# Optimization experiments

Hardware: AMD Instinct MI355X
Metric: run time of the kernel (lower is better)

Reference implementation:

```python
import jax, jax.numpy as jnp
import numpy as np

LOG2PI = float(np.log(2.0 * np.pi))


def setup_inputs() -> dict:
    key = jax.random.key(0)
    ks = jax.random.split(key, 5)
    B, T, XD, C = 128, 2050, 6, 64
    return {
        "x": jax.random.normal(ks[0], (B, T, XD), jnp.float32),
        "observation_means": jax.random.uniform(ks[1], (C, XD), dtype=jnp.float32),
        "observation_stddevs": jax.random.uniform(ks[2], (C, XD), dtype=jnp.float32),
        "log_A": jax.random.normal(ks[3], (C, C), jnp.float32),
        "log_pi": jax.random.normal(ks[4], (C,), jnp.float32),
    }


def _emission_logprob(x, means, stds):
    # Normal(means[:, :4], relu(stds[:, :4]) + 0.1).log_prob(x[:, :, :4]) summed over feat dim
    mu = means[:, :4]                       # (C,4)
    sigma = jax.nn.relu(stds[:, :4]) + 0.1  # (C,4)
    z = (x[:, :, None, :4] - mu) / sigma    # (B,T,C,4)
    return jnp.sum(-0.5 * z * z - jnp.log(sigma) - 0.5 * LOG2PI, axis=-1)  # (B,T,C)


def _forward_scalers(logp, log_A, log_pi):
    # scaled HMM forward pass; returns per-step log normalizers (T,B)
    a0 = logp[:, 0] + log_pi
    s0 = jax.nn.logsumexp(a0, axis=-1)
    a0n = a0 - s0[:, None]

    def step(a_prev, lp_t):
        a = lp_t + jax.nn.logsumexp(a_prev[:, :, None] + log_A[None], axis=1)
        s = jax.nn.logsumexp(a, axis=-1)
        return a - s[:, None], s

    _, s_rest = jax.lax.scan(step, a0n, jnp.swapaxes(logp[:, 1:], 0, 1))
    return jnp.concatenate([s0[None], s_rest], axis=0)  # (T,B)


def _viterbi(logp, log_A, log_pi):
    d0 = logp[:, 0] + log_pi  # (B,C)

    def step(d_prev, lp_t):
        scores = d_prev[:, :, None] + log_A[None]  # (B,C_prev,C_cur)
        psi_t = jnp.argmax(scores, axis=1)
        d = jnp.max(scores, axis=1) + lp_t
        return d, psi_t

    d_last, psi = jax.lax.scan(step, d0, jnp.swapaxes(logp[:, 1:], 0, 1))  # psi: (T-1,B,C)
    c_last = jnp.argmax(d_last, axis=-1)  # (B,)

    def back(c_next, psi_t):
        c_t = jnp.take_along_axis(psi_t, c_next[:, None], axis=1)[:, 0]
        return c_t, c_t

    _, cs = jax.lax.scan(back, c_last, psi, reverse=True)  # (T-1,B)
    c = jnp.concatenate([cs, c_last[None]], axis=0)  # (T,B)
    return jnp.swapaxes(c, 0, 1)  # (B,T)


def reference(x, observation_means, observation_stddevs, log_A, log_pi):
    logA = jax.nn.log_softmax(log_A, axis=1)
    logpi = jax.nn.log_softmax(log_pi, axis=0)
    logp = _emission_logprob(x, observation_means, observation_stddevs)  # (B,T,C)
    scalers = _forward_scalers(logp, logA, logpi)                         # (T,B)
    logp_x = jnp.sum(scalers, axis=0)                                     # (B,)
    c_est = _viterbi(logp, logA, logpi)                                   # (B,T) int
    return logp_x, c_est
```

## Files before the change

### kernel.cpp

```cpp
#include <hip/hip_runtime.h>

#define T_LEN 2050
#define B_SZ 128
#define NCHUNK 33
#define HL2PI 0.91893853320467274178f

__device__ __forceinline__ float waveMax(float v) {
#pragma unroll
    for (int off = 32; off >= 1; off >>= 1)
        v = fmaxf(v, __shfl_xor(v, off, 64));
    return v;
}
__device__ __forceinline__ float waveSum(float v) {
#pragma unroll
    for (int off = 32; off >= 1; off >>= 1)
        v += __shfl_xor(v, off, 64);
    return v;
}
__device__ __forceinline__ void waveArgmax(float& v, int& idx) {
#pragma unroll
    for (int off = 32; off >= 1; off >>= 1) {
        float ov = __shfl_xor(v, off, 64);
        int   oi = __shfl_xor(idx, off, 64);
        if (ov > v || (ov == v && oi < idx)) { v = ov; idx = oi; }
    }
}
__device__ __forceinline__ void cfence() { asm volatile("" ::: "memory"); }

__device__ __forceinline__ float rl(float v, int lane) {
    return __int_as_float(__builtin_amdgcn_readlane(__float_as_int(v), lane));
}

__device__ __forceinline__ float dppSumAll(float v) {
#define SSTEP(ctrl) { int t_ = __builtin_amdgcn_update_dpp(0, __float_as_int(v), ctrl, 0xf, 0xf, true); \
                      v = v + __int_as_float(t_); }
    SSTEP(0x111) SSTEP(0x112) SSTEP(0x114) SSTEP(0x118) SSTEP(0x142) SSTEP(0x143)
#undef SSTEP
    return __int_as_float(__builtin_amdgcn_readlane(__float_as_int(v), 63));
}
__device__ __forceinline__ float dppMaxAll(float v) {
#define MSTEP(ctrl) { int t_ = __builtin_amdgcn_update_dpp(__float_as_int(v), __float_as_int(v), ctrl, 0xf, 0xf, false); \
                      v = fmaxf(v, __int_as_float(t_)); }
    MSTEP(0x111) MSTEP(0x112) MSTEP(0x114) MSTEP(0x118) MSTEP(0x142) MSTEP(0x143)
#undef MSTEP
    return __int_as_float(__builtin_amdgcn_readlane(__float_as_int(v), 63));
}

extern "C" __global__ __launch_bounds__(64, 1)
void hmm_prep(const float* __restrict__ logA_in,
              const float* __restrict__ logpi_in,
              float* __restrict__ lAg,
              float* __restrict__ lpig)
{
    __shared__ float la[64 * 65];
    __shared__ float rowlse[64];
    const int j = threadIdx.x;
#pragma unroll
    for (int k = 0; k < 64; ++k)
        la[k * 65 + j] = logA_in[k * 64 + j];
    cfence();
    {
        float m = -1e30f;
#pragma unroll
        for (int k = 0; k < 64; ++k) m = fmaxf(m, la[j * 65 + k]);
        float s = 0.f;
#pragma unroll
        for (int k = 0; k < 64; ++k) s += expf(la[j * 65 + k] - m);
        rowlse[j] = m + logf(s);
    }
    cfence();
    {
        float v = logpi_in[j];
        float m = waveMax(v);
        float s = waveSum(expf(v - m));
        lpig[j] = v - (m + logf(s));
    }
    float4* o = (float4*)lAg;
#pragma unroll
    for (int k = 0; k < 16; ++k) {
        float4 v;
        v.x = la[(4 * k + 0) * 65 + j] - rowlse[4 * k + 0];
        v.y = la[(4 * k + 1) * 65 + j] - rowlse[4 * k + 1];
        v.z = la[(4 * k + 2) * 65 + j] - rowlse[4 * k + 2];
        v.w = la[(4 * k + 3) * 65 + j] - rowlse[4 * k + 3];
        o[j * 16 + k] = v;
    }
}

extern "C" __global__ __launch_bounds__(256)
void hmm_emis(const float* __restrict__ x,
              const float* __restrict__ means,
              const float* __restrict__ stds,
              float* __restrict__ buf,
              float* __restrict__ m_pre)
{
    const int wid = blockIdx.x * 4 + (threadIdx.x >> 6);
    const int j = threadIdx.x & 63;
    const int t = wid >> 7;
    const int b = wid & 127;

    const float* xt = x + ((size_t)b * T_LEN + t) * 6;
    float x0 = xt[0], x1 = xt[1], x2 = xt[2], x3 = xt[3];

    float mu0 = means[j * 6 + 0], mu1 = means[j * 6 + 1];
    float mu2 = means[j * 6 + 2], mu3 = means[j * 6 + 3];
    float sg0 = fmaxf(stds[j * 6 + 0], 0.f) + 0.1f;
    float sg1 = fmaxf(stds[j * 6 + 1], 0.f) + 0.1f;
    float sg2 = fmaxf(stds[j * 6 + 2], 0.f) + 0.1f;
    float sg3 = fmaxf(stds[j * 6 + 3], 0.f) + 0.1f;
    float ls0 = logf(sg0), ls1 = logf(sg1), ls2 = logf(sg2), ls3 = logf(sg3);

    float z0 = (x0 - mu0) / sg0, z1 = (x1 - mu1) / sg1;
    float z2 = (x2 - mu2) / sg2, z3 = (x3 - mu3) / sg3;
    float e0 = ((-0.5f * z0) * z0 - ls0) - HL2PI;
    float e1 = ((-0.5f * z1) * z1 - ls1) - HL2PI;
    float e2 = ((-0.5f * z2) * z2 - ls2) - HL2PI;
    float e3 = ((-0.5f * z3) * z3 - ls3) - HL2PI;
    float lp = ((e0 + e1) + e2) + e3;

    buf[((size_t)b * T_LEN + t) * 64 + j] = lp;
    float mm = waveMax(lp);
    if (j == 0) m_pre[(size_t)b * T_LEN + t] = mm;
}

#define VIT_REDUCE(SRC)                                                   \
    float m0 = -3.4e38f, m1 = -3.4e38f, m2 = -3.4e38f, m3 = -3.4e38f;     \
    _Pragma("unroll")                                                     \
    for (int gq = 0; gq < 4; ++gq) {                                      \
        float s_[16];                                                     \
        _Pragma("unroll")                                                 \
        for (int m_ = 0; m_ < 16; ++m_) s_[m_] = rl((SRC), 16 * gq + m_); \
        __builtin_amdgcn_sched_barrier(0);                                \
        _Pragma("unroll")                                                 \
        for (int k2 = 0; k2 < 4; k2 += 2) {                               \
            const int ia = 16 * gq + 4 * k2;                              \
            const int ib = ia + 4;                                        \
            float a0_ = s_[4*k2+0] + lA[ia+0], b0_ = s_[4*k2+4] + lA[ib+0]; \
            float a1_ = s_[4*k2+1] + lA[ia+1], b1_ = s_[4*k2+5] + lA[ib+1]; \
            float a2_ = s_[4*k2+2] + lA[ia+2], b2_ = s_[4*k2+6] + lA[ib+2]; \
            float a3_ = s_[4*k2+3] + lA[ia+3], b3_ = s_[4*k2+7] + lA[ib+3]; \
            m0 = fmaxf(fmaxf(m0, a0_), b0_);                              \
            m1 = fmaxf(fmaxf(m1, a1_), b1_);                              \
            m2 = fmaxf(fmaxf(m2, a2_), b2_);                              \
            m3 = fmaxf(fmaxf(m3, a3_), b3_);                              \
        }                                                                 \
    }

extern "C" __global__ __launch_bounds__(64, 1)
void hmm_main(const float* __restrict__ x,
              const float* __restrict__ means,
              const float* __restrict__ stds,
              const float* __restrict__ lAg,
              const float* __restrict__ lpig,
              float* __restrict__ out,
              float* __restrict__ buf,
              const float* __restrict__ m_pre,
              int* __restrict__ c_last)
{
    __shared__ __align__(16) float xs[12304];

    const int j   = threadIdx.x;
    const int bid = blockIdx.x;
    const bool is_fwd = (bid < B_SZ);
    const int b = is_fwd ? bid : bid - B_SZ;

    float lpi = lpig[j];

    if (is_fwd) {
        {
            const float4* xg4 = (const float4*)(x + (size_t)b * T_LEN * 6);
            float4* xs4 = (float4*)xs;
            for (int i = j; i < 3075; i += 64) xs4[i] = xg4[i];
        }
        float mu0 = means[j * 6 + 0], mu1 = means[j * 6 + 1];
        float mu2 = means[j * 6 + 2], mu3 = means[j * 6 + 3];
        float sg0 = fmaxf(stds[j * 6 + 0], 0.f) + 0.1f;
        float sg1 = fmaxf(stds[j * 6 + 1], 0.f) + 0.1f;
        float sg2 = fmaxf(stds[j * 6 + 2], 0.f) + 0.1f;
        float sg3 = fmaxf(stds[j * 6 + 3], 0.f) + 0.1f;
        float ls0 = logf(sg0), ls1 = logf(sg1), ls2 = logf(sg2), ls3 = logf(sg3);
        float i0 = 1.f / sg0, i1 = 1.f / sg1, i2 = 1.f / sg2, i3 = 1.f / sg3;
        float cst = -(ls0 + ls1 + ls2 + ls3) - 4.f * HL2PI;

        float Ac[64];
        {
            const float4* g = (const float4*)lAg;
#pragma unroll
            for (int k = 0; k < 16; ++k) {
                float4 v = g[j * 16 + k];
                Ac[4 * k + 0] = __expf(v.x); Ac[4 * k + 1] = __expf(v.y);
                Ac[4 * k + 2] = __expf(v.z); Ac[4 * k + 3] = __expf(v.w);
            }
        }
        cfence();

        float z0 = (xs[0] - mu0) * i0, z1 = (xs[1] - mu1) * i1;
        float z2 = (xs[2] - mu2) * i2, z3 = (xs[3] - mu3) * i3;
        float a0 = (cst - 0.5f * (z0 * z0 + z1 * z1 + z2 * z2 + z3 * z3)) + lpi;
        float m0a = dppMaxAll(a0);
        float u = __expf(a0 - m0a);
        float s0 = dppSumAll(u);
        double acc = (double)(m0a + __logf(s0));
        u *= (1.0f / s0);

        const float* mp = m_pre + (size_t)b * T_LEN;
        float g0 = mp[1], g1 = mp[2], g2 = mp[3], g3 = mp[4];

#pragma unroll 1
        for (int t = 1; t < T_LEN; ++t) {
            float mm_c = g0; g0 = g1; g1 = g2; g2 = g3;
            int tp = t + 4; if (tp > T_LEN - 1) tp = T_LEN - 1;
            g3 = mp[tp];

            int o = t * 6;
            float y0 = xs[o], y1 = xs[o + 1], y2 = xs[o + 2], y3 = xs[o + 3];
            float w0 = (y0 - mu0) * i0, w1 = (y1 - mu1) * i1;
            float w2 = (y2 - mu2) * i2, w3 = (y3 - mu3) * i3;
            float lp = cst - 0.5f * (w0 * w0 + w1 * w1 + w2 * w2 + w3 * w3);
            float e_c = __expf(lp - mm_c);

            float q0 = 0.f, q1 = 0.f, q2 = 0.f, q3 = 0.f;
#pragma unroll
            for (int gq = 0; gq < 4; ++gq) {
                float s[16];
#pragma unroll
                for (int m = 0; m < 16; ++m) s[m] = rl(u, 16 * gq + m);
#pragma unroll
                for (int k2 = 0; k2 < 4; ++k2) {
                    const int i = 16 * gq + 4 * k2;
                    q0 = fmaf(s[4 * k2 + 0], Ac[i + 0], q0);
                    q1 = fmaf(s[4 * k2 + 1], Ac[i + 1], q1);
                    q2 = fmaf(s[4 * k2 + 2], Ac[i + 2], q2);
                    q3 = fmaf(s[4 * k2 + 3], Ac[i + 3], q3);
                }
            }
            u = ((q0 + q1) + (q2 + q3)) * e_c;
            acc += (double)mm_c;
            if ((t & 3) == 0) {
                float ss = dppSumAll(u);
                acc += (double)__logf(ss);
                u *= (1.0f / ss);
            }
        }
        float sf = dppSumAll(u);
        acc += (double)__logf(sf);
        if (j == 0) out[b] = (float)acc;
    } else {
        float lA[64];
        {
            const float4* g = (const float4*)lAg;
#pragma unroll
            for (int k = 0; k < 16; ++k) {
                float4 v = g[j * 16 + k];
                lA[4 * k + 0] = v.x; lA[4 * k + 1] = v.y;
                lA[4 * k + 2] = v.z; lA[4 * k + 3] = v.w;
            }
        }
        float* bb = buf + (size_t)b * T_LEN * 64 + j;

        float dn = bb[0] + lpi;
        float lr[8];
#pragma unroll
        for (int i = 0; i < 8; ++i) lr[i] = bb[(size_t)(1 + i) * 64];
        bb[0] = dn;

#pragma unroll 1
        for (int tb = 1; tb <= 2033; tb += 8) {
#pragma unroll
            for (int q = 0; q < 8; ++q) {
                const int t = tb + q;
                float lp_c = lr[q];
                lr[q] = bb[(size_t)(t + 8) * 64];
                VIT_REDUCE(dn);
                dn = fmaxf(fmaxf(m0, m1), fmaxf(m2, m3)) + lp_c;
                bb[(size_t)t * 64] = dn;
            }
        }
        float l_last = bb[(size_t)2049 * 64];
#pragma unroll
        for (int q = 0; q < 8; ++q) {
            const int t = 2041 + q;
            float lp_c = lr[q];
            VIT_REDUCE(dn);
            dn = fmaxf(fmaxf(m0, m1), fmaxf(m2, m3)) + lp_c;
            bb[(size_t)t * 64] = dn;
        }
        {
            float lp_c = l_last;
            VIT_REDUCE(dn);
            dn = fmaxf(fmaxf(m0, m1), fmaxf(m2, m3)) + lp_c;
        }

        float vv = dn; int idx = j;
        waveArgmax(vv, idx);
        if (j == 0) c_last[b] = idx;
    }
}

extern "C" __global__ __launch_bounds__(256)
void hmm_psi(const float* __restrict__ buf,
             const float* __restrict__ lAg,
             unsigned char* __restrict__ psi)
{
    __shared__ __align__(16) float sd[4][64];
    const int warp = threadIdx.x >> 6;
    const int j = threadIdx.x & 63;
    const int wid = blockIdx.x * 4 + warp;

    float lA[64];
    {
        const float4* g = (const float4*)lAg;
#pragma unroll
        for (int k = 0; k < 16; ++k) {
            float4 v = g[j * 16 + k];
            lA[4 * k + 0] = v.x; lA[4 * k + 1] = v.y;
            lA[4 * k + 2] = v.z; lA[4 * k + 3] = v.w;
        }
    }
    const float4* dv = (const float4*)sd[warp];
    const int NP = 2049 * B_SZ;

    for (int p = wid; p < NP; p += 8192) {
        const int t = (p >> 7) + 1;
        const int b = p & 127;
        float dval = buf[((size_t)b * T_LEN + (t - 1)) * 64 + j];
        sd[warp][j] = dval;

        float bv0 = -3.4e38f, bv1 = -3.4e38f, bv2 = -3.4e38f, bv3 = -3.4e38f;
        int bi0 = 0, bi1 = 1, bi2 = 2, bi3 = 3;
#pragma unroll
        for (int k = 0; k < 16; ++k) {
            float4 dd = dv[k];
            float v0 = dd.x + lA[4 * k + 0];
            float v1 = dd.y + lA[4 * k + 1];
            float v2 = dd.z + lA[4 * k + 2];
            float v3 = dd.w + lA[4 * k + 3];
            if (v0 > bv0) { bv0 = v0; bi0 = 4 * k + 0; }
            if (v1 > bv1) { bv1 = v1; bi1 = 4 * k + 1; }
            if (v2 > bv2) { bv2 = v2; bi2 = 4 * k + 2; }
            if (v3 > bv3) { bv3 = v3; bi3 = 4 * k + 3; }
        }
        float best = bv0; int bidx = bi0;
        if (bv1 > best || (bv1 == best && bi1 < bidx)) { best = bv1; bidx = bi1; }
        if (bv2 > best || (bv2 == best && bi2 < bidx)) { best = bv2; bidx = bi2; }
        if (bv3 > best || (bv3 == best && bi3 < bidx)) { best = bv3; bidx = bi3; }

        psi[((size_t)t * B_SZ + b) * 64 + j] = (unsigned char)bidx;
    }
}

extern "C" __global__ __launch_bounds__(256)
void hmm_compose(const unsigned char* __restrict__ psi,
                 unsigned char* __restrict__ mt)
{
    const int w = blockIdx.x * 4 + (threadIdx.x >> 6);
    const int j = threadIdx.x & 63;
    const int g = w % NCHUNK;
    const int b = w / NCHUNK;
    const int e = (g < NCHUNK - 1) ? g * 64 + 64 : (T_LEN - 1);
    int M = j;
    for (int t = e; t >= g * 64 + 1; --t)
        M = psi[((size_t)t * B_SZ + b) * 64 + M];
    mt[((size_t)g * B_SZ + b) * 64 + j] = (unsigned char)M;
}

extern "C" __global__ __launch_bounds__(64, 1)
void hmm_fill(const unsigned char* __restrict__ psi,
              const unsigned char* __restrict__ mt,
              const int* __restrict__ c_last,
              float* __restrict__ out)
{
    __shared__ int sb[NCHUNK];
    const int b = blockIdx.x;
    const int g = threadIdx.x;
    const int cl = c_last[b];
    if (g == 0) {
        int cur = cl;
        for (int q = NCHUNK - 1; q >= 0; --q) {
            cur = mt[((size_t)q * B_SZ + b) * 64 + cur];
            sb[q] = cur;
        }
    }
    cfence();
    float* oc = out + B_SZ + (size_t)b * T_LEN;
    if (g == NCHUNK) {
        oc[T_LEN - 1] = (float)cl;
    } else if (g < NCHUNK) {
        const int e = (g < NCHUNK - 1) ? g * 64 + 64 : (T_LEN - 1);
        int s = (g < NCHUNK - 1) ? sb[g + 1] : cl;
        for (int t = e; t >= g * 64 + 1; --t) {
            s = psi[((size_t)t * B_SZ + b) * 64 + s];
            oc[t - 1] = (float)s;
        }
    }
}

extern "C" void kernel_launch(void* const* d_in, const int* in_sizes, int n_in,
                              void* d_out, int out_size, void* d_ws, size_t ws_size,
                              hipStream_t stream)
{
    const float* x      = (const float*)d_in[0];
    const float* means  = (const float*)d_in[1];
    const float* stds   = (const float*)d_in[2];
    const float* logA   = (const float*)d_in[3];
    const float* logpi  = (const float*)d_in[4];
    float* out = (float*)d_out;

    char* base = (char*)d_ws;
    float*         buf   = (float*)base;
    unsigned char* psi   = (unsigned char*)(base + 67174400);
    float*         m_pre = (float*)(base + 67174400);
    unsigned char* mt    = (unsigned char*)(base + 83968000);
    int*           cl    = (int*)(base + 84238336);
    float*         lAg   = (float*)(base + 84238848);
    float*         lpig  = (float*)(base + 84255232);

    hipLaunchKernelGGL(hmm_prep, dim3(1), dim3(64), 0, stream, logA, logpi, lAg, lpig);
    hipLaunchKernelGGL(hmm_emis, dim3((T_LEN * B_SZ) / 4), dim3(256), 0, stream,
                       x, means, stds, buf, m_pre);
    hipLaunchKernelGGL(hmm_main, dim3(2 * B_SZ), dim3(64), 0, stream,
                       x, means, stds, lAg, lpig, out, buf, m_pre, cl);
    hipLaunchKernelGGL(hmm_psi, dim3(2048), dim3(256), 0, stream, buf, lAg, psi);
    hipLaunchKernelGGL(hmm_compose, dim3((NCHUNK * B_SZ) / 4), dim3(256), 0, stream, psi, mt);
    hipLaunchKernelGGL(hmm_fill, dim3(B_SZ), dim3(64), 0, stream, psi, mt, cl, out);
}
```

Baseline: 993.6 us.

## Replace dependent psi gathers with register prefetch and cross-lane permutes in backtrace

The backtrace compose and fill kernels no longer chase pointers through global memory. Each lane now prefetches its own coalesced psi row eight steps ahead and follows the chain with ds_bpermute or readlane, so the dependent global-load latency is taken off the critical path. Chunk-boundary resolution moves into a separate hmm_bound kernel that uses readlane over the composed maps. Fill is spread across one wave per chunk instead of one thread per chunk. This adds a kernel launch, and sbg reuses the start of the workspace buffer, which is no longer needed at that point.

```diff
diff --git a/kernel.cpp b/kernel.cpp
--- a/kernel.cpp
+++ b/kernel.cpp
@@ -357,41 +357,78 @@
     const int j = threadIdx.x & 63;
     const int g = w % NCHUNK;
     const int b = w / NCHUNK;
-    const int e = (g < NCHUNK - 1) ? g * 64 + 64 : (T_LEN - 1);
+    const int e  = (g < NCHUNK - 1) ? g * 64 + 64 : (T_LEN - 1);
+    const int t0 = g * 64 + 1;
+
     int M = j;
-    for (int t = e; t >= g * 64 + 1; --t)
-        M = psi[((size_t)t * B_SZ + b) * 64 + M];
+    int r[8];
+#pragma unroll
+    for (int i = 0; i < 8; ++i) {
+        int t = e - i;
+        r[i] = (t >= t0) ? (int)psi[((size_t)t * B_SZ + b) * 64 + j] : 0;
+    }
+#pragma unroll 1
+    for (int t = e; t >= t0; --t) {
+        const int q = (e - t) & 7;
+        int row = r[q];
+        int tn = t - 8;
+        r[q] = (tn >= t0) ? (int)psi[((size_t)tn * B_SZ + b) * 64 + j] : 0;
+        M = __builtin_amdgcn_ds_bpermute(M << 2, row);
+    }
     mt[((size_t)g * B_SZ + b) * 64 + j] = (unsigned char)M;
 }
 
 extern "C" __global__ __launch_bounds__(64, 1)
+void hmm_bound(const unsigned char* __restrict__ mt,
+               const int* __restrict__ c_last,
+               int* __restrict__ sbg)
+{
+    const int b = blockIdx.x;
+    const int j = threadIdx.x;
+    int rows[NCHUNK];
+#pragma unroll
+    for (int q = 0; q < NCHUNK; ++q)
+        rows[q] = (int)mt[((size_t)q * B_SZ + b) * 64 + j];
+    int cur = c_last[b];
+#pragma unroll
+    for (int q = NCHUNK - 1; q >= 0; --q) {
+        cur = __builtin_amdgcn_readlane(rows[q], cur);
+        if (j == 0) sbg[b * NCHUNK + q] = cur;
+    }
+}
+
+extern "C" __global__ __launch_bounds__(256)
 void hmm_fill(const unsigned char* __restrict__ psi,
-              const unsigned char* __restrict__ mt,
+              const int* __restrict__ sbg,
               const int* __restrict__ c_last,
               float* __restrict__ out)
 {
-    __shared__ int sb[NCHUNK];
-    const int b = blockIdx.x;
-    const int g = threadIdx.x;
+    const int w = blockIdx.x * 4 + (threadIdx.x >> 6);
+    const int j = threadIdx.x & 63;
+    const int g = w % NCHUNK;
+    const int b = w / NCHUNK;
     const int cl = c_last[b];
-    if (g == 0) {
-        int cur = cl;
-        for (int q = NCHUNK - 1; q >= 0; --q) {
-            cur = mt[((size_t)q * B_SZ + b) * 64 + cur];
-            sb[q] = cur;
-        }
-    }
-    cfence();
     float* oc = out + B_SZ + (size_t)b * T_LEN;
-    if (g == NCHUNK) {
-        oc[T_LEN - 1] = (float)cl;
-    } else if (g < NCHUNK) {
-        const int e = (g < NCHUNK - 1) ? g * 64 + 64 : (T_LEN - 1);
-        int s = (g < NCHUNK - 1) ? sb[g + 1] : cl;
-        for (int t = e; t >= g * 64 + 1; --t) {
-            s = psi[((size_t)t * B_SZ + b) * 64 + s];
-            oc[t - 1] = (float)s;
-        }
+
+    const int e  = (g < NCHUNK - 1) ? g * 64 + 64 : (T_LEN - 1);
+    const int t0 = g * 64 + 1;
+    int s = (g < NCHUNK - 1) ? sbg[b * NCHUNK + g + 1] : cl;
+    if (g == NCHUNK - 1 && j == 0) oc[T_LEN - 1] = (float)cl;
+
+    int r[8];
+#pragma unroll
+    for (int i = 0; i < 8; ++i) {
+        int t = e - i;
+        r[i] = (t >= t0) ? (int)psi[((size_t)t * B_SZ + b) * 64 + j] : 0;
+    }
+#pragma unroll 1
+    for (int t = e; t >= t0; --t) {
+        const int q = (e - t) & 7;
+        int row = r[q];
+        int tn = t - 8;
+        r[q] = (tn >= t0) ? (int)psi[((size_t)tn * B_SZ + b) * 64 + j] : 0;
+        s = __builtin_amdgcn_readlane(row, s);
+        if (j == 0) oc[t - 1] = (float)s;
     }
 }
 
@@ -414,6 +451,7 @@
     int*           cl    = (int*)(base + 84238336);
     float*         lAg   = (float*)(base + 84238848);
     float*         lpig  = (float*)(base + 84255232);
+    int*           sbg   = (int*)base;
 
     hipLaunchKernelGGL(hmm_prep, dim3(1), dim3(64), 0, stream, logA, logpi, lAg, lpig);
     hipLaunchKernelGGL(hmm_emis, dim3((T_LEN * B_SZ) / 4), dim3(256), 0, stream,
@@ -422,5 +460,6 @@
                        x, means, stds, lAg, lpig, out, buf, m_pre, cl);
     hipLaunchKernelGGL(hmm_psi, dim3(2048), dim3(256), 0, stream, buf, lAg, psi);
     hipLaunchKernelGGL(hmm_compose, dim3((NCHUNK * B_SZ) / 4), dim3(256), 0, stream, psi, mt);
-    hipLaunchKernelGGL(hmm_fill, dim3(B_SZ), dim3(64), 0, stream, psi, mt, cl, out);
-}
+    hipLaunchKernelGGL(hmm_bound, dim3(B_SZ), dim3(64), 0, stream, mt, cl, sbg);
+    hipLaunchKernelGGL(hmm_fill, dim3((NCHUNK * B_SZ) / 4), dim3(256), 0, stream, psi, sbg, cl, out);
+}
```

Result: slower. 1.018 ms (+2.5%).

## Fuse prep into emission kernel and psi computation into chunk composition

Applied to the files above, without the earlier changes.

The logA/logpi normalization moves into block 0 of the emission kernel, which removes one launch. The psi argmax kernel and the chunk composition kernel become a single kernel: each wave handles one (batch, chunk), computes psi for its 64 timesteps, and keeps them in shared memory so the backward composition reads LDS instead of walking global memory. This cuts two launches and the dependent global-memory chain in compose. In exchange, psi work is spread over only 4224 waves with a serial inner loop, and 16KB of extra LDS per block may lower occupancy.

```diff
diff --git a/kernel.cpp b/kernel.cpp
--- a/kernel.cpp
+++ b/kernel.cpp
@@ -46,54 +46,20 @@
     return __int_as_float(__builtin_amdgcn_readlane(__float_as_int(v), 63));
 }
 
-extern "C" __global__ __launch_bounds__(64, 1)
-void hmm_prep(const float* __restrict__ logA_in,
+extern "C" __global__ __launch_bounds__(256)
+void hmm_emis(const float* __restrict__ x,
+              const float* __restrict__ means,
+              const float* __restrict__ stds,
+              float* __restrict__ buf,
+              float* __restrict__ m_pre,
+              const float* __restrict__ logA_in,
               const float* __restrict__ logpi_in,
               float* __restrict__ lAg,
               float* __restrict__ lpig)
 {
     __shared__ float la[64 * 65];
     __shared__ float rowlse[64];
-    const int j = threadIdx.x;
-#pragma unroll
-    for (int k = 0; k < 64; ++k)
-        la[k * 65 + j] = logA_in[k * 64 + j];
-    cfence();
-    {
-        float m = -1e30f;
-#pragma unroll
-        for (int k = 0; k < 64; ++k) m = fmaxf(m, la[j * 65 + k]);
-        float s = 0.f;
-#pragma unroll
-        for (int k = 0; k < 64; ++k) s += expf(la[j * 65 + k] - m);
-        rowlse[j] = m + logf(s);
-    }
-    cfence();
-    {
-        float v = logpi_in[j];
-        float m = waveMax(v);
-        float s = waveSum(expf(v - m));
-        lpig[j] = v - (m + logf(s));
-    }
-    float4* o = (float4*)lAg;
-#pragma unroll
-    for (int k = 0; k < 16; ++k) {
-        float4 v;
-        v.x = la[(4 * k + 0) * 65 + j] - rowlse[4 * k + 0];
-        v.y = la[(4 * k + 1) * 65 + j] - rowlse[4 * k + 1];
-        v.z = la[(4 * k + 2) * 65 + j] - rowlse[4 * k + 2];
-        v.w = la[(4 * k + 3) * 65 + j] - rowlse[4 * k + 3];
-        o[j * 16 + k] = v;
-    }
-}
-
-extern "C" __global__ __launch_bounds__(256)
-void hmm_emis(const float* __restrict__ x,
-              const float* __restrict__ means,
-              const float* __restrict__ stds,
-              float* __restrict__ buf,
-              float* __restrict__ m_pre)
-{
+
     const int wid = blockIdx.x * 4 + (threadIdx.x >> 6);
     const int j = threadIdx.x & 63;
     const int t = wid >> 7;
@@ -121,6 +87,39 @@
     buf[((size_t)b * T_LEN + t) * 64 + j] = lp;
     float mm = waveMax(lp);
     if (j == 0) m_pre[(size_t)b * T_LEN + t] = mm;
+
+    if (blockIdx.x == 0 && threadIdx.x < 64) {
+#pragma unroll
+        for (int k = 0; k < 64; ++k)
+            la[k * 65 + j] = logA_in[k * 64 + j];
+        cfence();
+        {
+            float m = -1e30f;
+#pragma unroll
+            for (int k = 0; k < 64; ++k) m = fmaxf(m, la[j * 65 + k]);
+            float s = 0.f;
+#pragma unroll
+            for (int k = 0; k < 64; ++k) s += expf(la[j * 65 + k] - m);
+            rowlse[j] = m + logf(s);
+        }
+        cfence();
+        {
+            float v = logpi_in[j];
+            float m = waveMax(v);
+            float s = waveSum(expf(v - m));
+            lpig[j] = v - (m + logf(s));
+        }
+        float4* o = (float4*)lAg;
+#pragma unroll
+        for (int k = 0; k < 16; ++k) {
+            float4 v;
+            v.x = la[(4 * k + 0) * 65 + j] - rowlse[4 * k + 0];
+            v.y = la[(4 * k + 1) * 65 + j] - rowlse[4 * k + 1];
+            v.z = la[(4 * k + 2) * 65 + j] - rowlse[4 * k + 2];
+            v.w = la[(4 * k + 3) * 65 + j] - rowlse[4 * k + 3];
+            o[j * 16 + k] = v;
+        }
+    }
 }
 
 #define VIT_REDUCE(SRC)                                                   \
@@ -298,31 +297,36 @@
 }
 
 extern "C" __global__ __launch_bounds__(256)
-void hmm_psi(const float* __restrict__ buf,
-             const float* __restrict__ lAg,
-             unsigned char* __restrict__ psi)
+void hmm_pscomp(const float* __restrict__ buf,
+                const float* __restrict__ lAg,
+                unsigned char* __restrict__ psi,
+                unsigned char* __restrict__ mt)
 {
     __shared__ __align__(16) float sd[4][64];
+    __shared__ unsigned char prow[4][64][64];
+
     const int warp = threadIdx.x >> 6;
     const int j = threadIdx.x & 63;
-    const int wid = blockIdx.x * 4 + warp;
+    const int w = blockIdx.x * 4 + warp;
+    const int g = w % NCHUNK;
+    const int b = w / NCHUNK;
+    const int t0 = g * 64 + 1;
+    const int e  = (g < NCHUNK - 1) ? g * 64 + 64 : (T_LEN - 1);
 
     float lA[64];
     {
-        const float4* g = (const float4*)lAg;
+        const float4* gp = (const float4*)lAg;
 #pragma unroll
         for (int k = 0; k < 16; ++k) {
-            float4 v = g[j * 16 + k];
+            float4 v = gp[j * 16 + k];
             lA[4 * k + 0] = v.x; lA[4 * k + 1] = v.y;
             lA[4 * k + 2] = v.z; lA[4 * k + 3] = v.w;
         }
     }
     const float4* dv = (const float4*)sd[warp];
-    const int NP = 2049 * B_SZ;
-
-    for (int p = wid; p < NP; p += 8192) {
-        const int t = (p >> 7) + 1;
-        const int b = p & 127;
+
+#pragma unroll 1
+    for (int t = t0; t <= e; ++t) {
         float dval = buf[((size_t)b * T_LEN + (t - 1)) * 64 + j];
         sd[warp][j] = dval;
 
@@ -346,21 +350,13 @@
         if (bv3 > best || (bv3 == best && bi3 < bidx)) { best = bv3; bidx = bi3; }
 
         psi[((size_t)t * B_SZ + b) * 64 + j] = (unsigned char)bidx;
-    }
-}
-
-extern "C" __global__ __launch_bounds__(256)
-void hmm_compose(const unsigned char* __restrict__ psi,
-                 unsigned char* __restrict__ mt)
-{
-    const int w = blockIdx.x * 4 + (threadIdx.x >> 6);
-    const int j = threadIdx.x & 63;
-    const int g = w % NCHUNK;
-    const int b = w / NCHUNK;
-    const int e = (g < NCHUNK - 1) ? g * 64 + 64 : (T_LEN - 1);
+        prow[warp][t - t0][j] = (unsigned char)bidx;
+    }
+
     int M = j;
-    for (int t = e; t >= g * 64 + 1; --t)
-        M = psi[((size_t)t * B_SZ + b) * 64 + M];
+#pragma unroll 1
+    for (int tr = e - t0; tr >= 0; --tr)
+        M = (int)prow[warp][tr][M];
     mt[((size_t)g * B_SZ + b) * 64 + j] = (unsigned char)M;
 }
 
@@ -415,12 +411,11 @@
     float*         lAg   = (float*)(base + 84238848);
     float*         lpig  = (float*)(base + 84255232);
 
-    hipLaunchKernelGGL(hmm_prep, dim3(1), dim3(64), 0, stream, logA, logpi, lAg, lpig);
     hipLaunchKernelGGL(hmm_emis, dim3((T_LEN * B_SZ) / 4), dim3(256), 0, stream,
-                       x, means, stds, buf, m_pre);
+                       x, means, stds, buf, m_pre, logA, logpi, lAg, lpig);
     hipLaunchKernelGGL(hmm_main, dim3(2 * B_SZ), dim3(64), 0, stream,
                        x, means, stds, lAg, lpig, out, buf, m_pre, cl);
-    hipLaunchKernelGGL(hmm_psi, dim3(2048), dim3(256), 0, stream, buf, lAg, psi);
-    hipLaunchKernelGGL(hmm_compose, dim3((NCHUNK * B_SZ) / 4), dim3(256), 0, stream, psi, mt);
+    hipLaunchKernelGGL(hmm_pscomp, dim3((NCHUNK * B_SZ) / 4), dim3(256), 0, stream,
+                       buf, lAg, psi, mt);
     hipLaunchKernelGGL(hmm_fill, dim3(B_SZ), dim3(64), 0, stream, psi, mt, cl, out);
 }
```

Result: no change. 1.010 ms (+1.6%).
